# Performance work log

Measured on AMD Instinct MI355X. Metric: run time of the kernel, lower is better.

Reference implementation:

```python
import jax, jax.numpy as jnp
import numpy as np

HEAD_DIM = 64
NUM_HEADS = 16
ROPE_BASE = 10000.0


def _rope_cos_sin(seq_len, head_dim, dtype):
    inv_freq = 1.0 / (ROPE_BASE ** (jnp.arange(0, head_dim, 2, dtype=jnp.float32) / head_dim))
    t = jnp.arange(seq_len, dtype=jnp.float32)
    freqs = jnp.outer(t, inv_freq)                      # [S, D/2]
    emb = jnp.concatenate([freqs, freqs], axis=-1)      # [S, D]
    return jnp.cos(emb).astype(dtype), jnp.sin(emb).astype(dtype)


def _rotate_half(x):
    x1, x2 = jnp.split(x, 2, axis=-1)
    return jnp.concatenate([-x2, x1], axis=-1)


def setup_inputs() -> dict:
    key = jax.random.key(0)
    ks = jax.random.split(key, 5)
    B, S, H = 2, 2048, 1024
    x = jax.random.normal(ks[0], (B, S, H), dtype=jnp.float32)
    attention_mask = jnp.ones((B, S), dtype=jnp.float32)
    scale = 0.02
    Wq = jax.random.normal(ks[1], (H, H), dtype=jnp.float32) * scale
    Wk = jax.random.normal(ks[2], (H, H), dtype=jnp.float32) * scale
    Wv = jax.random.normal(ks[3], (H, H), dtype=jnp.float32) * scale
    Wo = jax.random.normal(ks[4], (H, H), dtype=jnp.float32) * scale
    return {"x": x, "attention_mask": attention_mask, "Wq": Wq, "Wk": Wk, "Wv": Wv, "Wo": Wo}


def reference(x, attention_mask, Wq, Wk, Wv, Wo):
    B, S, H = x.shape
    nh, hd = NUM_HEADS, HEAD_DIM
    scale = hd ** -0.5

    # nn.Linear semantics: y = x @ W^T  (W is [out, in])
    q = jnp.einsum('bsh,oh->bso', x, Wq).reshape(B, S, nh, hd).transpose(0, 2, 1, 3)
    k = jnp.einsum('bsh,oh->bso', x, Wk).reshape(B, S, nh, hd).transpose(0, 2, 1, 3)
    v = jnp.einsum('bsh,oh->bso', x, Wv).reshape(B, S, nh, hd).transpose(0, 2, 1, 3)

    cos, sin = _rope_cos_sin(S, hd, x.dtype)            # [S, hd]
    cos = cos[None, None, :, :]
    sin = sin[None, None, :, :]
    q = q * cos + _rotate_half(q) * sin
    k = k * cos + _rotate_half(k) * sin

    attn = jnp.einsum('bhqd,bhkd->bhqk', q, k) * scale  # [B, nh, S, S]
    mask = (1.0 - attention_mask.astype(x.dtype))[:, None, None, :] * jnp.finfo(x.dtype).min
    attn = attn + mask
    attn = jax.nn.softmax(attn, axis=-1)
    out = jnp.einsum('bhqk,bhkd->bhqd', attn, v)        # [B, nh, S, hd]
    out = out.transpose(0, 2, 1, 3).reshape(B, S, nh * hd)
    return jnp.einsum('bso,ho->bsh', out, Wo)
```

## Files before the change

### kernel.cpp

```cpp
#include <hip/hip_runtime.h>
#include <math.h>

#define BB 2
#define SS 2048
#define HH 1024
#define NH 16
#define HD 64
#define MM (BB*SS)

typedef __attribute__((ext_vector_type(8))) _Float16 f16x8;
typedef __attribute__((ext_vector_type(2))) __fp16 hf16x2;
typedef __attribute__((ext_vector_type(4))) float f32x4;

#define QSCALE 0.18033688011112042f

__device__ __forceinline__ unsigned short f2h(float f) {
    union { _Float16 h; unsigned short u; } c;
    c.h = (_Float16)f;
    return c.u;
}

__device__ __forceinline__ unsigned int pkh(float a, float b) {
    union { hf16x2 h; unsigned int u; } c;
    c.h = __builtin_amdgcn_cvt_pkrtz(a, b);
    return c.u;
}

__device__ __forceinline__ void gld16(const void* g, void* s) {
    __builtin_amdgcn_global_load_lds(
        (const __attribute__((address_space(1))) void*)g,
        (__attribute__((address_space(3))) void*)s, 16, 0, 0);
}

__global__ __launch_bounds__(256) void prep(
    const float* __restrict__ x, const float* __restrict__ mask,
    const float* __restrict__ Wq, const float* __restrict__ Wk,
    const float* __restrict__ Wv, const float* __restrict__ Wo,
    unsigned short* __restrict__ xf, unsigned short* __restrict__ wf,
    float* __restrict__ ctab, float* __restrict__ stab, float* __restrict__ mt)
{
    int gtid = blockIdx.x * 256 + threadIdx.x;
    if (gtid < SS * 32) {
        int s = gtid >> 5, i = gtid & 31;
        double invf = pow(10000.0, -(double)i / 32.0);
        double a = (double)s * invf;
        ctab[gtid] = (float)cos(a);
        stab[gtid] = (float)sin(a);
    }
    if (gtid < BB * SS)
        mt[gtid] = (1.0f - mask[gtid]) * (-1.0e38f);
    for (int it = gtid; it < 2097152; it += 524288) {
        float4 v; unsigned short* d; size_t off;
        if (it < 1048576) {
            off = (size_t)it * 4;
            v = *(const float4*)(x + off);
            d = xf;
        } else {
            off = (size_t)(it - 1048576) * 4;
            int row = (int)(off >> 10);
            const float* W = row < 1024 ? Wq : row < 2048 ? Wk : row < 3072 ? Wv : Wo;
            v = *(const float4*)(W + (((size_t)(row & 1023)) << 10) + (off & 1023));
            d = wf;
        }
        *(ushort4*)(d + off) = make_ushort4(f2h(v.x), f2h(v.y), f2h(v.z), f2h(v.w));
    }
}

template<int MODE>
__global__ __launch_bounds__(256, 3) void gemm3(
    const unsigned short* __restrict__ Axf,
    const unsigned short* __restrict__ Wf,
    const float* __restrict__ ctab, const float* __restrict__ stab,
    unsigned short* __restrict__ qo, unsigned short* __restrict__ ko,
    unsigned short* __restrict__ vo, float* __restrict__ fout)
{
    __shared__ __align__(16) short lsA[2][128*32];
    __shared__ __align__(16) short lsB[2][128*32];

    const int t = threadIdx.x;
    const int m0 = blockIdx.x * 128;
    const int brow0 = (MODE == 0 ? 0 : 3072) + blockIdx.y * 128;
    const int lane = t & 63, wv = t >> 6;
    const int wm = (wv >> 1) * 64, wn = (wv & 1) * 64;
    const int fr = lane & 15, fg = lane >> 4;

    const int srow = t >> 2, pc = t & 3;
    const int scx = (pc ^ ((srow >> 1) & 3)) * 8;
    const int lo  = srow * 32 + pc * 8;
    const size_t gA0 = (size_t)(m0 + srow) * HH + scx;
    const size_t gA1 = (size_t)(m0 + 64 + srow) * HH + scx;
    const size_t gB0 = (size_t)(brow0 + srow) * HH + scx;
    const size_t gB1 = (size_t)(brow0 + 64 + srow) * HH + scx;

    f32x4 acc[4][4] = {};

#define STAGE(sel, kk) do { \
        gld16(Axf + gA0 + (kk), &lsA[sel][lo]);            \
        gld16(Wf  + gB0 + (kk), &lsB[sel][lo]);            \
        gld16(Axf + gA1 + (kk), &lsA[sel][lo + 64*32]);    \
        gld16(Wf  + gB1 + (kk), &lsB[sel][lo + 64*32]);    \
    } while (0)

    STAGE(0, 0);
    __syncthreads();

    int cur = 0;
    for (int k0 = 0; k0 < HH; k0 += 32) {
        if (k0 + 32 < HH) STAGE(cur ^ 1, k0 + 32);

        f16x8 ah[4], bh[4];
        const int swz = (fg ^ ((fr >> 1) & 3)) * 8;
        #pragma unroll
        for (int mi = 0; mi < 4; ++mi)
            ah[mi] = *(const f16x8*)&lsA[cur][(wm + 16*mi + fr)*32 + swz];
        #pragma unroll
        for (int ni = 0; ni < 4; ++ni)
            bh[ni] = *(const f16x8*)&lsB[cur][(wn + 16*ni + fr)*32 + swz];

        __builtin_amdgcn_s_setprio(1);
        #pragma unroll
        for (int mi = 0; mi < 4; ++mi)
            #pragma unroll
            for (int ni = 0; ni < 4; ++ni)
                acc[mi][ni] = __builtin_amdgcn_mfma_f32_16x16x32_f16(ah[mi], bh[ni], acc[mi][ni], 0, 0, 0);
        __builtin_amdgcn_s_setprio(0);
        __syncthreads();
        cur ^= 1;
    }
#undef STAGE

    if (MODE == 0) {
        const int mat = brow0 >> 10;
        const int obase = (brow0 & 1023) + wn;
        const int h = obase >> 6;
        #pragma unroll
        for (int mi = 0; mi < 4; ++mi)
            #pragma unroll
            for (int rr = 0; rr < 4; ++rr) {
                int m = m0 + wm + 16*mi + 4*fg + rr;
                int b = m >> 11, s = m & (SS - 1);
                float v[4];
                #pragma unroll
                for (int ni = 0; ni < 4; ++ni) v[ni] = acc[mi][ni][rr];
                if (mat < 2) {
                    #pragma unroll
                    for (int ni = 0; ni < 2; ++ni) {
                        int i = 16*ni + fr;
                        float c = ctab[s*32 + i], sn = stab[s*32 + i];
                        float v1 = v[ni], v2 = v[ni + 2];
                        v[ni]     = v1*c - v2*sn;
                        v[ni + 2] = v2*c + v1*sn;
                    }
                }
                if (mat == 0) {
                    #pragma unroll
                    for (int ni = 0; ni < 4; ++ni) v[ni] *= QSCALE;
                }
                size_t base = ((size_t)(b*NH + h) * SS + s) * HD;
                #pragma unroll
                for (int ni = 0; ni < 4; ++ni) {
                    int d = 16*ni + fr;
                    unsigned short hb = f2h(v[ni]);
                    if (mat == 0)      qo[base + d] = hb;
                    else if (mat == 1) ko[base + (d ^ ((s & 7) << 3))] = hb;
                    else {
                        size_t va = ((size_t)(b*NH + h) * HD + d) * SS
                                  + (s & ~63) + ((s & 63) ^ ((d & 7) << 3));
                        vo[va] = hb;
                    }
                }
            }
    } else {
        const int n0 = blockIdx.y * 128 + wn;
        #pragma unroll
        for (int mi = 0; mi < 4; ++mi)
            #pragma unroll
            for (int rr = 0; rr < 4; ++rr) {
                int m = m0 + wm + 16*mi + 4*fg + rr;
                #pragma unroll
                for (int ni = 0; ni < 4; ++ni)
                    fout[(size_t)m * HH + n0 + 16*ni + fr] = acc[mi][ni][rr];
            }
    }
}

__global__ __launch_bounds__(512, 2) void attn(
    const unsigned short* __restrict__ qg, const unsigned short* __restrict__ kg,
    const unsigned short* __restrict__ vtg, const float* __restrict__ mt,
    unsigned short* __restrict__ cf)
{
    __shared__ __align__(16) short Ks[2][64*64];
    __shared__ __align__(16) short Vs[2][64*64];
    __shared__ __align__(16) short Ps[128*64];

    const int t = threadIdx.x, lane = t & 63, wv = t >> 6;
    const int fr = lane & 15, fg = lane >> 4, frx = fr & 7;
    const int bh = blockIdx.y, b = bh >> 4, h = bh & 15;
    const int q0 = blockIdx.x * 128;

    const unsigned short* kgb = kg  + (size_t)bh*SS*HD;
    const unsigned short* vgb = vtg + (size_t)bh*HD*SS;
    const float* mtb = mt + (size_t)b*SS;

    f16x8 qa[2];
    #pragma unroll
    for (int kc = 0; kc < 2; ++kc)
        qa[kc] = *(const f16x8*)&qg[((size_t)bh*SS + q0 + 16*wv + fr)*HD + kc*32 + fg*8];

    f32x4 o[4] = {};
    float lpart = 0.f;
    const int pbase = (wv*16 + fr) * 64;

    const int srow = t >> 3, sg = t & 7;

    gld16(kgb + (size_t)srow*HD + sg*8, &Ks[0][srow*64 + sg*8]);
    gld16(vgb + (size_t)srow*SS + sg*8, &Vs[0][srow*64 + sg*8]);
    __syncthreads();

    int cur = 0;
    for (int kt = 0; kt < SS/64; ++kt) {
        const int k0 = kt * 64;
        if (kt + 1 < SS/64) {
            const int kn = k0 + 64;
            gld16(kgb + (size_t)(kn+srow)*HD + sg*8, &Ks[cur^1][srow*64 + sg*8]);
            gld16(vgb + (size_t)srow*SS + kn + sg*8, &Vs[cur^1][srow*64 + sg*8]);
        }

        float4 m4[4];
        #pragma unroll
        for (int nf = 0; nf < 4; ++nf)
            m4[nf] = *(const float4*)&mtb[k0 + 16*nf + 4*fg];

        f32x4 sc[4] = {};
        __builtin_amdgcn_s_setprio(1);
        #pragma unroll
        for (int kc = 0; kc < 2; ++kc) {
            #pragma unroll
            for (int nf = 0; nf < 4; ++nf) {
                int gr = (4*kc + fg) ^ frx;
                f16x8 kb = *(const f16x8*)&Ks[cur][(16*nf + fr)*64 + gr*8];
                sc[nf] = __builtin_amdgcn_mfma_f32_16x16x32_f16(kb, qa[kc], sc[nf], 0, 0, 0);
            }
        }
        __builtin_amdgcn_s_setprio(0);

        #pragma unroll
        for (int nf = 0; nf < 4; ++nf) {
            float p0 = __builtin_amdgcn_exp2f(sc[nf][0] + m4[nf].x);
            float p1 = __builtin_amdgcn_exp2f(sc[nf][1] + m4[nf].y);
            float p2 = __builtin_amdgcn_exp2f(sc[nf][2] + m4[nf].z);
            float p3 = __builtin_amdgcn_exp2f(sc[nf][3] + m4[nf].w);
            lpart += (p0 + p1) + (p2 + p3);
            uint2 w; w.x = pkh(p0, p1); w.y = pkh(p2, p3);
            *(uint2*)&Ps[pbase + (((2*nf + (fg >> 1)) ^ frx) * 8) + 4*(fg & 1)] = w;
        }

        __builtin_amdgcn_s_setprio(1);
        #pragma unroll
        for (int kc = 0; kc < 2; ++kc) {
            int gr = (4*kc + fg) ^ frx;
            f16x8 pa = *(const f16x8*)&Ps[pbase + gr*8];
            #pragma unroll
            for (int df = 0; df < 4; ++df) {
                f16x8 vb = *(const f16x8*)&Vs[cur][(16*df + fr)*64 + gr*8];
                o[df] = __builtin_amdgcn_mfma_f32_16x16x32_f16(vb, pa, o[df], 0, 0, 0);
            }
        }
        __builtin_amdgcn_s_setprio(0);
        __syncthreads();
        cur ^= 1;
    }

    float l = lpart;
    l += __shfl_xor(l, 16);
    l += __shfl_xor(l, 32);
    float inv = 1.0f / l;
    size_t base = ((size_t)b*SS + q0 + 16*wv + fr)*HH + h*HD;
    #pragma unroll
    for (int df = 0; df < 4; ++df) {
        uint2 w;
        w.x = pkh(o[df][0]*inv, o[df][1]*inv);
        w.y = pkh(o[df][2]*inv, o[df][3]*inv);
        *(uint2*)&cf[base + 16*df + 4*fg] = w;
    }
}

extern "C" void kernel_launch(void* const* d_in, const int* in_sizes, int n_in,
                              void* d_out, int out_size, void* d_ws, size_t ws_size,
                              hipStream_t stream) {
    const float* x    = (const float*)d_in[0];
    const float* mask = (const float*)d_in[1];
    const float* Wq   = (const float*)d_in[2];
    const float* Wk   = (const float*)d_in[3];
    const float* Wv   = (const float*)d_in[4];
    const float* Wo   = (const float*)d_in[5];
    float* out = (float*)d_out;

    const size_t T = (size_t)MM * HH;
    unsigned short* xf = (unsigned short*)d_ws;
    unsigned short* wf = xf + T;
    unsigned short* qt = wf + T;
    unsigned short* kt = qt + T;
    unsigned short* vt = kt + T;
    float* ctab = (float*)(vt + T);
    float* stab = ctab + SS*32;
    float* mt   = stab + SS*32;
    unsigned short* cf = xf;

    prep<<<2048, 256, 0, stream>>>(x, mask, Wq, Wk, Wv, Wo, xf, wf, ctab, stab, mt);
    gemm3<0><<<dim3(MM/128, 3*HH/128), 256, 0, stream>>>(xf, wf, ctab, stab,
                                                         qt, kt, vt, nullptr);
    attn<<<dim3(SS/128, BB*NH), 512, 0, stream>>>(qt, kt, vt, mt, cf);
    gemm3<1><<<dim3(MM/128, HH/128), 256, 0, stream>>>(cf, wf, nullptr, nullptr,
                                                       nullptr, nullptr, nullptr, out);
}
```

Before: 121.6 us.

## Skip mask loads for unmasked key tiles, sum probabilities via MFMA, remap grid

Prep now records a per-64-key flag saying whether every mask entry in that tile is one. The attention kernel reads this flag and skips the mask load and add on fully unmasked tiles. The row sum of probabilities comes from an extra MFMA against a vector of ones instead of scalar adds plus shuffles. The grid is flattened and remapped so that neighbouring blocks share the same head's K/V, and the P buffer gets a padded stride. The extra MFMA per k-chunk and the larger shared-memory footprint add cost, and the row sum now accumulates the fp16-rounded probabilities.

```diff
diff --git a/kernel.cpp b/kernel.cpp
--- a/kernel.cpp
+++ b/kernel.cpp
@@ -37,7 +37,8 @@
     const float* __restrict__ Wq, const float* __restrict__ Wk,
     const float* __restrict__ Wv, const float* __restrict__ Wo,
     unsigned short* __restrict__ xf, unsigned short* __restrict__ wf,
-    float* __restrict__ ctab, float* __restrict__ stab, float* __restrict__ mt)
+    float* __restrict__ ctab, float* __restrict__ stab, float* __restrict__ mt,
+    unsigned int* __restrict__ mflag)
 {
     int gtid = blockIdx.x * 256 + threadIdx.x;
     if (gtid < SS * 32) {
@@ -47,8 +48,13 @@
         ctab[gtid] = (float)cos(a);
         stab[gtid] = (float)sin(a);
     }
-    if (gtid < BB * SS)
-        mt[gtid] = (1.0f - mask[gtid]) * (-1.0e38f);
+    if (gtid < BB * SS) {
+        float mv = mask[gtid];
+        mt[gtid] = (1.0f - mv) * (-1.0e38f);
+        unsigned long long bal = __ballot(mv == 1.0f);
+        if ((threadIdx.x & 63) == 0)
+            mflag[gtid >> 6] = (bal == ~0ull) ? 1u : 0u;
+    }
     for (int it = gtid; it < 2097152; it += 524288) {
         float4 v; unsigned short* d; size_t off;
         if (it < 1048576) {
@@ -187,29 +193,36 @@
 __global__ __launch_bounds__(512, 2) void attn(
     const unsigned short* __restrict__ qg, const unsigned short* __restrict__ kg,
     const unsigned short* __restrict__ vtg, const float* __restrict__ mt,
-    unsigned short* __restrict__ cf)
+    const unsigned int* __restrict__ mfl, unsigned short* __restrict__ cf)
 {
     __shared__ __align__(16) short Ks[2][64*64];
     __shared__ __align__(16) short Vs[2][64*64];
-    __shared__ __align__(16) short Ps[128*64];
+    __shared__ __align__(16) short Ps[128*72];
 
     const int t = threadIdx.x, lane = t & 63, wv = t >> 6;
     const int fr = lane & 15, fg = lane >> 4, frx = fr & 7;
-    const int bh = blockIdx.y, b = bh >> 4, h = bh & 15;
-    const int q0 = blockIdx.x * 128;
+    const int flat = blockIdx.x;
+    const int bh = (flat & 7) + ((flat >> 7) << 3);
+    const int q0 = ((flat >> 3) & 15) * 128;
+    const int b = bh >> 4, h = bh & 15;
 
     const unsigned short* kgb = kg  + (size_t)bh*SS*HD;
     const unsigned short* vgb = vtg + (size_t)bh*HD*SS;
     const float* mtb = mt + (size_t)b*SS;
+    const unsigned int* mfb = mfl + b*32;
 
     f16x8 qa[2];
     #pragma unroll
     for (int kc = 0; kc < 2; ++kc)
         qa[kc] = *(const f16x8*)&qg[((size_t)bh*SS + q0 + 16*wv + fr)*HD + kc*32 + fg*8];
 
+    f16x8 onev;
+    #pragma unroll
+    for (int i = 0; i < 8; ++i) onev[i] = (_Float16)1.0f;
+
     f32x4 o[4] = {};
-    float lpart = 0.f;
-    const int pbase = (wv*16 + fr) * 64;
+    f32x4 oS = {};
+    const int pbase = (wv*16 + fr) * 72;
 
     const int srow = t >> 3, sg = t & 7;
 
@@ -225,11 +238,7 @@
             gld16(kgb + (size_t)(kn+srow)*HD + sg*8, &Ks[cur^1][srow*64 + sg*8]);
             gld16(vgb + (size_t)srow*SS + kn + sg*8, &Vs[cur^1][srow*64 + sg*8]);
         }
-
-        float4 m4[4];
-        #pragma unroll
-        for (int nf = 0; nf < 4; ++nf)
-            m4[nf] = *(const float4*)&mtb[k0 + 16*nf + 4*fg];
+        const int fl = __builtin_amdgcn_readfirstlane(mfb[kt]);
 
         f32x4 sc[4] = {};
         __builtin_amdgcn_s_setprio(1);
@@ -244,15 +253,27 @@
         }
         __builtin_amdgcn_s_setprio(0);
 
-        #pragma unroll
-        for (int nf = 0; nf < 4; ++nf) {
-            float p0 = __builtin_amdgcn_exp2f(sc[nf][0] + m4[nf].x);
-            float p1 = __builtin_amdgcn_exp2f(sc[nf][1] + m4[nf].y);
-            float p2 = __builtin_amdgcn_exp2f(sc[nf][2] + m4[nf].z);
-            float p3 = __builtin_amdgcn_exp2f(sc[nf][3] + m4[nf].w);
-            lpart += (p0 + p1) + (p2 + p3);
-            uint2 w; w.x = pkh(p0, p1); w.y = pkh(p2, p3);
-            *(uint2*)&Ps[pbase + (((2*nf + (fg >> 1)) ^ frx) * 8) + 4*(fg & 1)] = w;
+        if (fl) {
+            #pragma unroll
+            for (int nf = 0; nf < 4; ++nf) {
+                float p0 = __builtin_amdgcn_exp2f(sc[nf][0]);
+                float p1 = __builtin_amdgcn_exp2f(sc[nf][1]);
+                float p2 = __builtin_amdgcn_exp2f(sc[nf][2]);
+                float p3 = __builtin_amdgcn_exp2f(sc[nf][3]);
+                uint2 w; w.x = pkh(p0, p1); w.y = pkh(p2, p3);
+                *(uint2*)&Ps[pbase + (((2*nf + (fg >> 1)) ^ frx) * 8) + 4*(fg & 1)] = w;
+            }
+        } else {
+            #pragma unroll
+            for (int nf = 0; nf < 4; ++nf) {
+                float4 m4 = *(const float4*)&mtb[k0 + 16*nf + 4*fg];
+                float p0 = __builtin_amdgcn_exp2f(sc[nf][0] + m4.x);
+                float p1 = __builtin_amdgcn_exp2f(sc[nf][1] + m4.y);
+                float p2 = __builtin_amdgcn_exp2f(sc[nf][2] + m4.z);
+                float p3 = __builtin_amdgcn_exp2f(sc[nf][3] + m4.w);
+                uint2 w; w.x = pkh(p0, p1); w.y = pkh(p2, p3);
+                *(uint2*)&Ps[pbase + (((2*nf + (fg >> 1)) ^ frx) * 8) + 4*(fg & 1)] = w;
+            }
         }
 
         __builtin_amdgcn_s_setprio(1);
@@ -265,16 +286,14 @@
                 f16x8 vb = *(const f16x8*)&Vs[cur][(16*df + fr)*64 + gr*8];
                 o[df] = __builtin_amdgcn_mfma_f32_16x16x32_f16(vb, pa, o[df], 0, 0, 0);
             }
+            oS = __builtin_amdgcn_mfma_f32_16x16x32_f16(onev, pa, oS, 0, 0, 0);
         }
         __builtin_amdgcn_s_setprio(0);
         __syncthreads();
         cur ^= 1;
     }
 
-    float l = lpart;
-    l += __shfl_xor(l, 16);
-    l += __shfl_xor(l, 32);
-    float inv = 1.0f / l;
+    float inv = 1.0f / oS[0];
     size_t base = ((size_t)b*SS + q0 + 16*wv + fr)*HH + h*HD;
     #pragma unroll
     for (int df = 0; df < 4; ++df) {
@@ -305,12 +324,13 @@
     float* ctab = (float*)(vt + T);
     float* stab = ctab + SS*32;
     float* mt   = stab + SS*32;
+    unsigned int* mfg = (unsigned int*)(mt + BB*SS);
     unsigned short* cf = xf;
 
-    prep<<<2048, 256, 0, stream>>>(x, mask, Wq, Wk, Wv, Wo, xf, wf, ctab, stab, mt);
+    prep<<<2048, 256, 0, stream>>>(x, mask, Wq, Wk, Wv, Wo, xf, wf, ctab, stab, mt, mfg);
     gemm3<0><<<dim3(MM/128, 3*HH/128), 256, 0, stream>>>(xf, wf, ctab, stab,
                                                          qt, kt, vt, nullptr);
-    attn<<<dim3(SS/128, BB*NH), 512, 0, stream>>>(qt, kt, vt, mt, cf);
+    attn<<<512, 512, 0, stream>>>(qt, kt, vt, mt, mfg, cf);
     gemm3<1><<<dim3(MM/128, HH/128), 256, 0, stream>>>(cf, wf, nullptr, nullptr,
                                                        nullptr, nullptr, nullptr, out);
 }
```

New measurement: 134.1 us. 1.1x slower.
